# Optimization experiments

Hardware: AMD Instinct MI355X
Metric: run time of the kernel (lower is better)

## Reference

```python
import jax, jax.numpy as jnp
import numpy as np

N_NODES = 50000
NEG_SLOPE = 0.2


def _gat_conv(x, src, dst, W, a_src, a_dst, b, num_nodes):
    # x: [N, F_in]; src/dst: [E'] (self-loops already appended)
    H, C = a_src.shape
    h = (x @ W).reshape(num_nodes, H, C)            # [N, H, C]
    al_s = (h * a_src).sum(-1)                      # [N, H]
    al_d = (h * a_dst).sum(-1)                      # [N, H]
    e = jax.nn.leaky_relu(al_s[src] + al_d[dst], NEG_SLOPE)  # [E', H]
    # segment softmax over incoming edges of each destination node
    e_max = jax.ops.segment_max(e, dst, num_segments=num_nodes)
    e_max = jnp.where(jnp.isfinite(e_max), e_max, 0.0)
    ex = jnp.exp(e - e_max[dst])
    denom = jax.ops.segment_sum(ex, dst, num_segments=num_nodes)
    alpha = ex / (denom[dst] + 1e-16)               # [E', H]
    msg = h[src] * alpha[:, :, None]                # [E', H, C]
    out = jax.ops.segment_sum(msg, dst, num_segments=num_nodes)  # [N, H, C]
    return out.reshape(num_nodes, H * C) + b


def _glorot(key, shape):
    fan_in, fan_out = shape[0], shape[-1]
    std = np.sqrt(2.0 / (fan_in + fan_out)).astype(np.float32)
    return jax.random.normal(key, shape, dtype=jnp.float32) * std


def setup_inputs() -> dict:
    key = jax.random.key(0)
    ks = jax.random.split(key, 16)
    N, F_in, Hid, Cls, H = N_NODES, 128, 128, 40, 8
    C = Hid // H  # 16
    inp = {
        "x": jax.random.normal(ks[0], (N, F_in), dtype=jnp.float32),
        "edge_index": jax.random.randint(ks[1], (2, 800000), 0, N, dtype=jnp.int32),
        # layer 0: F_in -> H x C
        "W0": _glorot(ks[2], (F_in, H * C)),
        "as0": _glorot(ks[3], (H, C)),
        "ad0": _glorot(ks[4], (H, C)),
        "b0": jnp.zeros((H * C,), dtype=jnp.float32),
        # layer 1: Hid -> H x C
        "W1": _glorot(ks[5], (Hid, H * C)),
        "as1": _glorot(ks[6], (H, C)),
        "ad1": _glorot(ks[7], (H, C)),
        "b1": jnp.zeros((H * C,), dtype=jnp.float32),
        "W2": _glorot(ks[8], (Hid, Cls)),
        "as2": _glorot(ks[9], (1, Cls)),
        "ad2": _glorot(ks[10], (1, Cls)),
        "b2": jnp.zeros((Cls,), dtype=jnp.float32),
    }
    return inp


def reference(x, edge_index, W0, as0, ad0, b0, W1, as1, ad1, b1, W2, as2, ad2, b2):
    N = x.shape[0]
    loop = jnp.arange(N, dtype=edge_index.dtype)
    src = jnp.concatenate([edge_index[0], loop])  # add self-loops (PyG default)
    dst = jnp.concatenate([edge_index[1], loop])
    h = _gat_conv(x, src, dst, W0, as0, ad0, b0, N)
    h = jax.nn.relu(h)                      # dropout is identity in eval mode
    h = _gat_conv(h, src, dst, W1, as1, ad1, b1, N)
    h = jax.nn.relu(h)
    out = _gat_conv(h, src, dst, W2, as2, ad2, b2, N)  # [N, n_classes]
    return out
```

## Files before the change

kernel.cpp:

```cpp
#include <hip/hip_runtime.h>

#define NN    50000
#define ERAW  800000
#define ETOT  850000
#define NBUCK 782
#define EBR   1280
#define EPB_A 4096
#define NBLK_A ((ETOT + EPB_A - 1) / EPB_A)
#define NCNT  (NBUCK * 64)

typedef __attribute__((ext_vector_type(8))) short bf16x8;
typedef __attribute__((ext_vector_type(4))) float f32x4;

union U16x8 { uint4 u; bf16x8 s; };
__device__ __forceinline__ bf16x8 as_bf(uint4 v) { U16x8 t; t.u = v; return t.s; }

__device__ __forceinline__ void edge_sd(const int* __restrict__ ei, int e, int& s, int& d) {
    if (e < ERAW) { s = ei[e]; d = ei[ERAW + e]; }
    else { int n = e - ERAW; s = n; d = n; }
}

__device__ __forceinline__ unsigned pack_bf16x2(float a, float b) {
    unsigned ua = __float_as_uint(a), ub = __float_as_uint(b);
    ua += 0x7fffu + ((ua >> 16) & 1u);
    ub += 0x7fffu + ((ub >> 16) & 1u);
    return (ua >> 16) | (ub & 0xffff0000u);
}
__device__ __forceinline__ float2 unpack_bf16x2(unsigned v) {
    float2 r;
    r.x = __uint_as_float(v << 16);
    r.y = __uint_as_float(v & 0xffff0000u);
    return r;
}

__global__ void prep_misc(const float* __restrict__ W0, const float* __restrict__ W1,
                          const float* __restrict__ W2,
                          const float* __restrict__ as0, const float* __restrict__ ad0,
                          const float* __restrict__ as1, const float* __restrict__ ad1,
                          const float* __restrict__ as2, const float* __restrict__ ad2,
                          unsigned* __restrict__ Wbp0, unsigned* __restrict__ Wbp1,
                          unsigned* __restrict__ Wadp0, unsigned* __restrict__ Wadp1,
                          float* __restrict__ W2e, int* __restrict__ cursor) {
    int g = blockIdx.x * 256 + threadIdx.x;
    if (g < 4096) {
        int which = g >> 11;
        int r = g & 2047;
        int ct = r >> 8, kc = (r >> 6) & 3, l = r & 63;
        int lr = l & 15, lg = l >> 4;
        int col = ct * 16 + lr, k0 = kc * 32 + lg * 8;
        const float* W = which ? W1 : W0;
        unsigned* O = which ? Wbp1 : Wbp0;
        uint4 o;
        o.x = pack_bf16x2(W[(k0 + 0) * 128 + col], W[(k0 + 1) * 128 + col]);
        o.y = pack_bf16x2(W[(k0 + 2) * 128 + col], W[(k0 + 3) * 128 + col]);
        o.z = pack_bf16x2(W[(k0 + 4) * 128 + col], W[(k0 + 5) * 128 + col]);
        o.w = pack_bf16x2(W[(k0 + 6) * 128 + col], W[(k0 + 7) * 128 + col]);
        ((uint4*)O)[(ct * 4 + kc) * 64 + l] = o;
    } else if (g < 4608) {
        int gg = g - 4096;
        int which = gg >> 8;
        int r = gg & 255;
        int kc = r >> 6, l = r & 63;
        int lr = l & 15, lg = l >> 4;
        const float* W = which ? W1 : W0;
        const float* av = (lr < 8) ? (which ? as1 : as0) : (which ? ad1 : ad0);
        unsigned* O = which ? Wadp1 : Wadp0;
        int h = lr & 7;
        int k0 = kc * 32 + lg * 8;
        float v[8];
        #pragma unroll
        for (int j = 0; j < 8; ++j) {
            float s = 0.f;
            #pragma unroll
            for (int c = 0; c < 16; ++c) s += W[(k0 + j) * 128 + h * 16 + c] * av[h * 16 + c];
            v[j] = s;
        }
        uint4 o;
        o.x = pack_bf16x2(v[0], v[1]);
        o.y = pack_bf16x2(v[2], v[3]);
        o.z = pack_bf16x2(v[4], v[5]);
        o.w = pack_bf16x2(v[6], v[7]);
        ((uint4*)O)[kc * 64 + l] = o;
    } else if (g < 4608 + 6144) {
        int gg = g - 4608;
        int k = gg / 48, j = gg - k * 48;
        float v = 0.f;
        if (j < 40) v = W2[k * 40 + j];
        else if (j == 40) { for (int c = 0; c < 40; ++c) v += W2[k * 40 + c] * as2[c]; }
        else if (j == 41) { for (int c = 0; c < 40; ++c) v += W2[k * 40 + c] * ad2[c]; }
        W2e[k * 48 + j] = v;
    } else if (g < 4608 + 6144 + NBUCK) {
        int b = g - 10752;
        cursor[b] = b * EBR;
    }
}

__global__ void conv_x(const float* __restrict__ x, unsigned* __restrict__ xb) {
    int g = blockIdx.x * 256 + threadIdx.x;
    if (g >= NN * 32) return;
    float4 v = ((const float4*)x)[g];
    uint2 o;
    o.x = pack_bf16x2(v.x, v.y);
    o.y = pack_bf16x2(v.z, v.w);
    ((uint2*)xb)[g] = o;
}

__global__ __launch_bounds__(256) void kA3(const int* __restrict__ ei, int* __restrict__ cursor,
                                           unsigned* __restrict__ ebkt) {
    __shared__ int lb[NBUCK];
    int t = threadIdx.x;
    for (int i = t; i < NBUCK; i += 256) lb[i] = 0;
    __syncthreads();
    int base = blockIdx.x * EPB_A;
    #pragma unroll 4
    for (int k = 0; k < EPB_A / 256; ++k) {
        int e = base + k * 256 + t;
        if (e < ETOT) {
            int s, d; edge_sd(ei, e, s, d); (void)s;
            atomicAdd(&lb[d >> 6], 1);
        }
    }
    __syncthreads();
    for (int i = t; i < NBUCK; i += 256) {
        int c = lb[i];
        lb[i] = c ? atomicAdd(&cursor[i], c) : 0;
    }
    __syncthreads();
    #pragma unroll 4
    for (int k = 0; k < EPB_A / 256; ++k) {
        int e = base + k * 256 + t;
        if (e < ETOT) {
            int s, d; edge_sd(ei, e, s, d);
            int b = d >> 6;
            int pos = atomicAdd(&lb[b], 1);
            if (pos < (b + 1) * EBR)
                ebkt[pos] = ((unsigned)d << 16) | (unsigned)s;
        }
    }
}

__global__ __launch_bounds__(256) void kB(const int* __restrict__ cursor,
                                          const unsigned* __restrict__ ebkt,
                                          int* __restrict__ row_start, int* __restrict__ row_end,
                                          unsigned short* __restrict__ src_u16) {
    __shared__ int lc[64];
    int b = blockIdx.x, t = threadIdx.x;
    if (t < 64) lc[t] = 0;
    __syncthreads();
    int s0 = b * EBR;
    int s1 = cursor[b]; if (s1 > s0 + EBR) s1 = s0 + EBR;
    for (int i = s0 + t; i < s1; i += 256) atomicAdd(&lc[(ebkt[i] >> 16) & 63], 1);
    __syncthreads();
    if (t < 64) {
        int v = lc[t];
        int inc = v;
        #pragma unroll
        for (int off = 1; off < 64; off <<= 1) {
            int u = __shfl_up(inc, off);
            if (t >= off) inc += u;
        }
        int st = s0 + inc - v;
        row_start[b * 64 + t] = st;
        row_end[b * 64 + t] = st + v;
        lc[t] = st;
    }
    __syncthreads();
    for (int i = s0 + t; i < s1; i += 256) {
        unsigned k = ebkt[i];
        int pos = atomicAdd(&lc[(k >> 16) & 63], 1);
        src_u16[pos] = (unsigned short)(k & 0xffffu);
    }
}

__global__ __launch_bounds__(256) void gemm_mfma128(
    const uint4* __restrict__ xb, const uint4* __restrict__ Wbp,
    const uint4* __restrict__ Wadp, unsigned* __restrict__ hb,
    float* __restrict__ als, float* __restrict__ ald)
{
    int t = threadIdx.x;
    int wv = t >> 6, l = t & 63;
    int lr = l & 15, lg = l >> 4;
    int n0 = blockIdx.x * 64 + wv * 16;
    int nodeA = n0 + lr; if (nodeA >= NN) nodeA = NN - 1;
    const uint4* xr = xb + (size_t)nodeA * 16;
    uint4 a0 = xr[0 * 4 + lg];
    uint4 a1 = xr[1 * 4 + lg];
    uint4 a2 = xr[2 * 4 + lg];
    uint4 a3 = xr[3 * 4 + lg];
    #pragma unroll
    for (int ct = 0; ct < 8; ++ct) {
        const uint4* bp = Wbp + (size_t)(ct * 4) * 64;
        uint4 b0 = bp[0 * 64 + l];
        uint4 b1 = bp[1 * 64 + l];
        uint4 b2 = bp[2 * 64 + l];
        uint4 b3 = bp[3 * 64 + l];
        f32x4 acc = {0.f, 0.f, 0.f, 0.f};
        acc = __builtin_amdgcn_mfma_f32_16x16x32_bf16(as_bf(a0), as_bf(b0), acc, 0, 0, 0);
        acc = __builtin_amdgcn_mfma_f32_16x16x32_bf16(as_bf(a1), as_bf(b1), acc, 0, 0, 0);
        acc = __builtin_amdgcn_mfma_f32_16x16x32_bf16(as_bf(a2), as_bf(b2), acc, 0, 0, 0);
        acc = __builtin_amdgcn_mfma_f32_16x16x32_bf16(as_bf(a3), as_bf(b3), acc, 0, 0, 0);
        #pragma unroll
        for (int j = 0; j < 4; ++j) {
            float hv = acc[j];
            float nbv = __shfl_xor(hv, 1);
            int node = n0 + lg * 4 + j;
            if ((lr & 1) == 0 && node < NN)
                hb[(size_t)node * 64 + ct * 8 + (lr >> 1)] = pack_bf16x2(hv, nbv);
        }
    }
    {
        uint4 b0 = Wadp[0 * 64 + l];
        uint4 b1 = Wadp[1 * 64 + l];
        uint4 b2 = Wadp[2 * 64 + l];
        uint4 b3 = Wadp[3 * 64 + l];
        f32x4 acc = {0.f, 0.f, 0.f, 0.f};
        acc = __builtin_amdgcn_mfma_f32_16x16x32_bf16(as_bf(a0), as_bf(b0), acc, 0, 0, 0);
        acc = __builtin_amdgcn_mfma_f32_16x16x32_bf16(as_bf(a1), as_bf(b1), acc, 0, 0, 0);
        acc = __builtin_amdgcn_mfma_f32_16x16x32_bf16(as_bf(a2), as_bf(b2), acc, 0, 0, 0);
        acc = __builtin_amdgcn_mfma_f32_16x16x32_bf16(as_bf(a3), as_bf(b3), acc, 0, 0, 0);
        #pragma unroll
        for (int j = 0; j < 4; ++j) {
            int node = n0 + lg * 4 + j;
            if (node < NN) {
                if (lr < 8) als[node * 8 + lr] = acc[j];
                else        ald[node * 8 + (lr - 8)] = acc[j];
            }
        }
    }
}

__global__ __launch_bounds__(256) void gemm_att40(
    const unsigned* __restrict__ fb, const float* __restrict__ W2e,
    unsigned* __restrict__ hb40, float* __restrict__ als, float* __restrict__ ald)
{
    __shared__ float ws[128 * 48];
    __shared__ unsigned xs[16 * 64];
    int t = threadIdx.x;
    int n0 = blockIdx.x * 16;
    #pragma unroll
    for (int i = 0; i < 6; ++i) ((float4*)ws)[i * 256 + t] = ((const float4*)W2e)[i * 256 + t];
    ((uint4*)xs)[t] = ((const uint4*)fb)[(size_t)n0 * 16 + t];
    __syncthreads();
    int w = t >> 6, c = t & 63;
    int cc = c < 42 ? c : 41;
    float acc[4] = {0.f, 0.f, 0.f, 0.f};
    #pragma unroll 4
    for (int kc = 0; kc < 32; ++kc) {
        float w0 = ws[(kc * 4 + 0) * 48 + cc];
        float w1 = ws[(kc * 4 + 1) * 48 + cc];
        float w2 = ws[(kc * 4 + 2) * 48 + cc];
        float w3 = ws[(kc * 4 + 3) * 48 + cc];
        #pragma unroll
        for (int i = 0; i < 4; ++i) {
            float2 f0 = unpack_bf16x2(xs[(4 * w + i) * 64 + kc * 2]);
            float2 f1 = unpack_bf16x2(xs[(4 * w + i) * 64 + kc * 2 + 1]);
            acc[i] = fmaf(f0.x, w0, acc[i]);
            acc[i] = fmaf(f0.y, w1, acc[i]);
            acc[i] = fmaf(f1.x, w2, acc[i]);
            acc[i] = fmaf(f1.y, w3, acc[i]);
        }
    }
    #pragma unroll
    for (int i = 0; i < 4; ++i) {
        int n = n0 + 4 * w + i;
        float nb = __shfl_xor(acc[i], 1);
        if ((c & 1) == 0 && c < 40) hb40[(size_t)n * 32 + (c >> 1)] = pack_bf16x2(acc[i], nb);
        if (c == 40) als[n] = acc[i];
        if (c == 41) ald[n] = acc[i];
    }
}

template<bool RELU>
__global__ void dst_agg128(const int* __restrict__ row_start, const int* __restrict__ row_end,
                           const unsigned short* __restrict__ src_u16,
                           const float* __restrict__ als, const float* __restrict__ ald,
                           const unsigned* __restrict__ hb, const float* __restrict__ bias,
                           unsigned* __restrict__ outb)
{
    int wp = (blockIdx.x * blockDim.x + threadIdx.x) >> 6;
    if (wp >= NN / 4) return;
    int lane = threadIdx.x & 63;
    int q = lane >> 4, l = lane & 15;
    int node = 4 * wp + q;
    int myh = l >> 1;
    float aldv = ald[node * 8 + myh];
    int i = row_start[node], end = row_end[node];
    float4 accA = make_float4(0.f, 0.f, 0.f, 0.f);
    float4 accB = make_float4(0.f, 0.f, 0.f, 0.f);
    float den = 0.f;
    while (__any(i + 4 <= end)) {
        if (i + 4 <= end) {
            int s0 = src_u16[i], s1 = src_u16[i + 1], s2 = src_u16[i + 2], s3 = src_u16[i + 3];
            float e0 = als[s0 * 8 + myh] + aldv;
            float e1 = als[s1 * 8 + myh] + aldv;
            float e2 = als[s2 * 8 + myh] + aldv;
            float e3 = als[s3 * 8 + myh] + aldv;
            uint4 p0 = ((const uint4*)(hb + (size_t)s0 * 64))[l];
            uint4 p1 = ((const uint4*)(hb + (size_t)s1 * 64))[l];
            uint4 p2 = ((const uint4*)(hb + (size_t)s2 * 64))[l];
            uint4 p3 = ((const uint4*)(hb + (size_t)s3 * 64))[l];
            e0 = e0 > 0.f ? e0 : 0.2f * e0;
            e1 = e1 > 0.f ? e1 : 0.2f * e1;
            e2 = e2 > 0.f ? e2 : 0.2f * e2;
            e3 = e3 > 0.f ? e3 : 0.2f * e3;
            float a0 = __expf(e0), a1 = __expf(e1), a2 = __expf(e2), a3 = __expf(e3);
            den += (a0 + a1) + (a2 + a3);
            float2 t0, t1;
            t0 = unpack_bf16x2(p0.x); t1 = unpack_bf16x2(p0.y);
            accA.x = fmaf(t0.x, a0, accA.x); accA.y = fmaf(t0.y, a0, accA.y);
            accA.z = fmaf(t1.x, a0, accA.z); accA.w = fmaf(t1.y, a0, accA.w);
            t0 = unpack_bf16x2(p0.z); t1 = unpack_bf16x2(p0.w);
            accB.x = fmaf(t0.x, a0, accB.x); accB.y = fmaf(t0.y, a0, accB.y);
            accB.z = fmaf(t1.x, a0, accB.z); accB.w = fmaf(t1.y, a0, accB.w);
            t0 = unpack_bf16x2(p1.x); t1 = unpack_bf16x2(p1.y);
            accA.x = fmaf(t0.x, a1, accA.x); accA.y = fmaf(t0.y, a1, accA.y);
            accA.z = fmaf(t1.x, a1, accA.z); accA.w = fmaf(t1.y, a1, accA.w);
            t0 = unpack_bf16x2(p1.z); t1 = unpack_bf16x2(p1.w);
            accB.x = fmaf(t0.x, a1, accB.x); accB.y = fmaf(t0.y, a1, accB.y);
            accB.z = fmaf(t1.x, a1, accB.z); accB.w = fmaf(t1.y, a1, accB.w);
            t0 = unpack_bf16x2(p2.x); t1 = unpack_bf16x2(p2.y);
            accA.x = fmaf(t0.x, a2, accA.x); accA.y = fmaf(t0.y, a2, accA.y);
            accA.z = fmaf(t1.x, a2, accA.z); accA.w = fmaf(t1.y, a2, accA.w);
            t0 = unpack_bf16x2(p2.z); t1 = unpack_bf16x2(p2.w);
            accB.x = fmaf(t0.x, a2, accB.x); accB.y = fmaf(t0.y, a2, accB.y);
            accB.z = fmaf(t1.x, a2, accB.z); accB.w = fmaf(t1.y, a2, accB.w);
            t0 = unpack_bf16x2(p3.x); t1 = unpack_bf16x2(p3.y);
            accA.x = fmaf(t0.x, a3, accA.x); accA.y = fmaf(t0.y, a3, accA.y);
            accA.z = fmaf(t1.x, a3, accA.z); accA.w = fmaf(t1.y, a3, accA.w);
            t0 = unpack_bf16x2(p3.z); t1 = unpack_bf16x2(p3.w);
            accB.x = fmaf(t0.x, a3, accB.x); accB.y = fmaf(t0.y, a3, accB.y);
            accB.z = fmaf(t1.x, a3, accB.z); accB.w = fmaf(t1.y, a3, accB.w);
            i += 4;
        }
    }
    while (__any(i < end)) {
        if (i < end) {
            int s0 = src_u16[i];
            float e0 = als[s0 * 8 + myh] + aldv;
            e0 = e0 > 0.f ? e0 : 0.2f * e0;
            float a0 = __expf(e0);
            den += a0;
            uint4 p0 = ((const uint4*)(hb + (size_t)s0 * 64))[l];
            float2 t0 = unpack_bf16x2(p0.x), t1 = unpack_bf16x2(p0.y);
            accA.x = fmaf(t0.x, a0, accA.x); accA.y = fmaf(t0.y, a0, accA.y);
            accA.z = fmaf(t1.x, a0, accA.z); accA.w = fmaf(t1.y, a0, accA.w);
            t0 = unpack_bf16x2(p0.z); t1 = unpack_bf16x2(p0.w);
            accB.x = fmaf(t0.x, a0, accB.x); accB.y = fmaf(t0.y, a0, accB.y);
            accB.z = fmaf(t1.x, a0, accB.z); accB.w = fmaf(t1.y, a0, accB.w);
            ++i;
        }
    }
    float inv = 1.f / (den + 1e-16f);
    float4 bvA = ((const float4*)bias)[2 * l];
    float4 bvB = ((const float4*)bias)[2 * l + 1];
    float4 oA, oB;
    oA.x = accA.x * inv + bvA.x; oA.y = accA.y * inv + bvA.y;
    oA.z = accA.z * inv + bvA.z; oA.w = accA.w * inv + bvA.w;
    oB.x = accB.x * inv + bvB.x; oB.y = accB.y * inv + bvB.y;
    oB.z = accB.z * inv + bvB.z; oB.w = accB.w * inv + bvB.w;
    if (RELU) {
        oA.x = fmaxf(oA.x, 0.f); oA.y = fmaxf(oA.y, 0.f);
        oA.z = fmaxf(oA.z, 0.f); oA.w = fmaxf(oA.w, 0.f);
        oB.x = fmaxf(oB.x, 0.f); oB.y = fmaxf(oB.y, 0.f);
        oB.z = fmaxf(oB.z, 0.f); oB.w = fmaxf(oB.w, 0.f);
    }
    uint4 ob;
    ob.x = pack_bf16x2(oA.x, oA.y);
    ob.y = pack_bf16x2(oA.z, oA.w);
    ob.z = pack_bf16x2(oB.x, oB.y);
    ob.w = pack_bf16x2(oB.z, oB.w);
    ((uint4*)(outb + (size_t)node * 64))[l] = ob;
}

__global__ void dst_agg40(const int* __restrict__ row_start, const int* __restrict__ row_end,
                          const unsigned short* __restrict__ src_u16,
                          const float* __restrict__ als, const float* __restrict__ ald,
                          const unsigned* __restrict__ hb40, const float* __restrict__ bias,
                          float* __restrict__ out)
{
    int wp = (blockIdx.x * blockDim.x + threadIdx.x) >> 6;
    if (wp >= NN / 4) return;
    int lane = threadIdx.x & 63;
    int q = lane >> 4, l = lane & 15;
    int node = 4 * wp + q;
    float aldv = ald[node];
    int i = row_start[node], end = row_end[node];
    float4 acc = make_float4(0.f, 0.f, 0.f, 0.f);
    float den = 0.f;
    while (__any(i + 4 <= end)) {
        if (i + 4 <= end) {
            int s0 = src_u16[i], s1 = src_u16[i + 1], s2 = src_u16[i + 2], s3 = src_u16[i + 3];
            float e0 = als[s0] + aldv;
            float e1 = als[s1] + aldv;
            float e2 = als[s2] + aldv;
            float e3 = als[s3] + aldv;
            uint2 p0 = ((const uint2*)(hb40 + (size_t)s0 * 32))[l];
            uint2 p1 = ((const uint2*)(hb40 + (size_t)s1 * 32))[l];
            uint2 p2 = ((const uint2*)(hb40 + (size_t)s2 * 32))[l];
            uint2 p3 = ((const uint2*)(hb40 + (size_t)s3 * 32))[l];
            e0 = e0 > 0.f ? e0 : 0.2f * e0;
            e1 = e1 > 0.f ? e1 : 0.2f * e1;
            e2 = e2 > 0.f ? e2 : 0.2f * e2;
            e3 = e3 > 0.f ? e3 : 0.2f * e3;
            float b0 = __expf(e0), b1 = __expf(e1), b2 = __expf(e2), b3 = __expf(e3);
            den += (b0 + b1) + (b2 + b3);
            float2 u0 = unpack_bf16x2(p0.x), v0 = unpack_bf16x2(p0.y);
            float2 u1 = unpack_bf16x2(p1.x), v1 = unpack_bf16x2(p1.y);
            float2 u2 = unpack_bf16x2(p2.x), v2 = unpack_bf16x2(p2.y);
            float2 u3 = unpack_bf16x2(p3.x), v3 = unpack_bf16x2(p3.y);
            acc.x = fmaf(u0.x, b0, acc.x); acc.y = fmaf(u0.y, b0, acc.y);
            acc.z = fmaf(v0.x, b0, acc.z); acc.w = fmaf(v0.y, b0, acc.w);
            acc.x = fmaf(u1.x, b1, acc.x); acc.y = fmaf(u1.y, b1, acc.y);
            acc.z = fmaf(v1.x, b1, acc.z); acc.w = fmaf(v1.y, b1, acc.w);
            acc.x = fmaf(u2.x, b2, acc.x); acc.y = fmaf(u2.y, b2, acc.y);
            acc.z = fmaf(v2.x, b2, acc.z); acc.w = fmaf(v2.y, b2, acc.w);
            acc.x = fmaf(u3.x, b3, acc.x); acc.y = fmaf(u3.y, b3, acc.y);
            acc.z = fmaf(v3.x, b3, acc.z); acc.w = fmaf(v3.y, b3, acc.w);
            i += 4;
        }
    }
    while (__any(i < end)) {
        if (i < end) {
            int s0 = src_u16[i];
            float e0 = als[s0] + aldv;
            e0 = e0 > 0.f ? e0 : 0.2f * e0;
            float b0 = __expf(e0);
            den += b0;
            uint2 p0 = ((const uint2*)(hb40 + (size_t)s0 * 32))[l];
            float2 u0 = unpack_bf16x2(p0.x), v0 = unpack_bf16x2(p0.y);
            acc.x = fmaf(u0.x, b0, acc.x); acc.y = fmaf(u0.y, b0, acc.y);
            acc.z = fmaf(v0.x, b0, acc.z); acc.w = fmaf(v0.y, b0, acc.w);
            ++i;
        }
    }
    if (l < 10) {
        float inv = 1.f / (den + 1e-16f);
        float4 bv = ((const float4*)bias)[l];
        float4 o;
        o.x = acc.x * inv + bv.x;
        o.y = acc.y * inv + bv.y;
        o.z = acc.z * inv + bv.z;
        o.w = acc.w * inv + bv.w;
        ((float4*)(out + (size_t)node * 40))[l] = o;
    }
}

extern "C" void kernel_launch(void* const* d_in, const int* in_sizes, int n_in,
                              void* d_out, int out_size, void* d_ws, size_t ws_size,
                              hipStream_t stream) {
    const float* x   = (const float*)d_in[0];
    const int*   ei  = (const int*)d_in[1];
    const float* W0  = (const float*)d_in[2];
    const float* as0 = (const float*)d_in[3];
    const float* ad0 = (const float*)d_in[4];
    const float* b0  = (const float*)d_in[5];
    const float* W1  = (const float*)d_in[6];
    const float* as1 = (const float*)d_in[7];
    const float* ad1 = (const float*)d_in[8];
    const float* b1  = (const float*)d_in[9];
    const float* W2  = (const float*)d_in[10];
    const float* as2 = (const float*)d_in[11];
    const float* ad2 = (const float*)d_in[12];
    const float* b2  = (const float*)d_in[13];
    float* out = (float*)d_out;

    float* ws = (float*)d_ws;
    size_t off = 0;
    unsigned* hb   = (unsigned*)(ws + off); off += (size_t)NN * 64;
    unsigned* xb   = (unsigned*)(ws + off); off += (size_t)NN * 64;
    unsigned* fAb  = (unsigned*)(ws + off); off += (size_t)NN * 64;
    unsigned* fBb  = (unsigned*)(ws + off); off += (size_t)NN * 64;
    unsigned* hb40 = (unsigned*)(ws + off); off += (size_t)NN * 32;
    float* als     = ws + off; off += (size_t)NN * 8;
    float* ald     = ws + off; off += (size_t)NN * 8;
    unsigned* Wbp0 = (unsigned*)(ws + off); off += 8192;
    unsigned* Wbp1 = (unsigned*)(ws + off); off += 8192;
    unsigned* Wadp0 = (unsigned*)(ws + off); off += 1024;
    unsigned* Wadp1 = (unsigned*)(ws + off); off += 1024;
    float* W2e     = ws + off; off += 128 * 48;
    int* ibase      = (int*)(ws + off);
    int* cursor     = ibase; ibase += NBUCK;
    int* row_start  = ibase; ibase += NCNT;
    int* row_end    = ibase; ibase += NCNT;
    unsigned* ebkt  = (unsigned*)ibase; ibase += NBUCK * EBR;
    unsigned short* src_u16 = (unsigned short*)ibase;

    const int TB = 256;

    prep_misc<<<46, 256, 0, stream>>>(W0, W1, W2, as0, ad0, as1, ad1, as2, ad2,
                                      Wbp0, Wbp1, Wadp0, Wadp1, W2e, cursor);
    kA3<<<NBLK_A, 256, 0, stream>>>(ei, cursor, ebkt);
    kB<<<NBUCK, 256, 0, stream>>>(cursor, ebkt, row_start, row_end, src_u16);
    conv_x<<<(NN * 32 + TB - 1) / TB, TB, 0, stream>>>(x, xb);

    const int GGM   = (NN + 63) / 64;
    const int GG40  = NN / 16;
    const int GAGG4 = ((NN / 4) * 64 + TB - 1) / TB;

    gemm_mfma128<<<GGM, 256, 0, stream>>>((const uint4*)xb, (const uint4*)Wbp0,
                                          (const uint4*)Wadp0, hb, als, ald);
    dst_agg128<true><<<GAGG4, TB, 0, stream>>>(row_start, row_end, src_u16, als, ald, hb, b0, fAb);

    gemm_mfma128<<<GGM, 256, 0, stream>>>((const uint4*)fAb, (const uint4*)Wbp1,
                                          (const uint4*)Wadp1, hb, als, ald);
    dst_agg128<true><<<GAGG4, TB, 0, stream>>>(row_start, row_end, src_u16, als, ald, hb, b1, fBb);

    gemm_att40<<<GG40, 256, 0, stream>>>(fBb, W2e, hb40, als, ald);
    dst_agg40<<<GAGG4, TB, 0, stream>>>(row_start, row_end, src_u16, als, ald, hb40, b2, out);
}
```

Measured before the change: 189.6 us.

## Split edges across half-waves in aggregation, fold log2e into attention weights, merge conv_x

```diff
diff --git a/kernel.cpp b/kernel.cpp
--- a/kernel.cpp
+++ b/kernel.cpp
@@ -8,6 +8,7 @@
 #define EPB_A 4096
 #define NBLK_A ((ETOT + EPB_A - 1) / EPB_A)
 #define NCNT  (NBUCK * 64)
+#define INV_LN2 1.4426950408889634f
 
 typedef __attribute__((ext_vector_type(8))) short bf16x8;
 typedef __attribute__((ext_vector_type(4))) float f32x4;
@@ -33,14 +34,26 @@
     return r;
 }
 
-__global__ void prep_misc(const float* __restrict__ W0, const float* __restrict__ W1,
+__global__ void prep_conv(const float* __restrict__ x,
+                          const float* __restrict__ W0, const float* __restrict__ W1,
                           const float* __restrict__ W2,
                           const float* __restrict__ as0, const float* __restrict__ ad0,
                           const float* __restrict__ as1, const float* __restrict__ ad1,
                           const float* __restrict__ as2, const float* __restrict__ ad2,
                           unsigned* __restrict__ Wbp0, unsigned* __restrict__ Wbp1,
                           unsigned* __restrict__ Wadp0, unsigned* __restrict__ Wadp1,
-                          float* __restrict__ W2e, int* __restrict__ cursor) {
+                          float* __restrict__ W2e, int* __restrict__ cursor,
+                          unsigned* __restrict__ xb) {
+    if (blockIdx.x >= 46) {
+        int g = (blockIdx.x - 46) * 256 + threadIdx.x;
+        if (g >= NN * 32) return;
+        float4 v = ((const float4*)x)[g];
+        uint2 o;
+        o.x = pack_bf16x2(v.x, v.y);
+        o.y = pack_bf16x2(v.z, v.w);
+        ((uint2*)xb)[g] = o;
+        return;
+    }
     int g = blockIdx.x * 256 + threadIdx.x;
     if (g < 4096) {
         int which = g >> 11;
@@ -73,7 +86,7 @@
             float s = 0.f;
             #pragma unroll
             for (int c = 0; c < 16; ++c) s += W[(k0 + j) * 128 + h * 16 + c] * av[h * 16 + c];
-            v[j] = s;
+            v[j] = s * INV_LN2;
         }
         uint4 o;
         o.x = pack_bf16x2(v[0], v[1]);
@@ -86,23 +99,13 @@
         int k = gg / 48, j = gg - k * 48;
         float v = 0.f;
         if (j < 40) v = W2[k * 40 + j];
-        else if (j == 40) { for (int c = 0; c < 40; ++c) v += W2[k * 40 + c] * as2[c]; }
-        else if (j == 41) { for (int c = 0; c < 40; ++c) v += W2[k * 40 + c] * ad2[c]; }
+        else if (j == 40) { for (int c = 0; c < 40; ++c) v += W2[k * 40 + c] * as2[c]; v *= INV_LN2; }
+        else if (j == 41) { for (int c = 0; c < 40; ++c) v += W2[k * 40 + c] * ad2[c]; v *= INV_LN2; }
         W2e[k * 48 + j] = v;
     } else if (g < 4608 + 6144 + NBUCK) {
         int b = g - 10752;
         cursor[b] = b * EBR;
     }
-}
-
-__global__ void conv_x(const float* __restrict__ x, unsigned* __restrict__ xb) {
-    int g = blockIdx.x * 256 + threadIdx.x;
-    if (g >= NN * 32) return;
-    float4 v = ((const float4*)x)[g];
-    uint2 o;
-    o.x = pack_bf16x2(v.x, v.y);
-    o.y = pack_bf16x2(v.z, v.w);
-    ((uint2*)xb)[g] = o;
 }
 
 __global__ __launch_bounds__(256) void kA3(const int* __restrict__ ei, int* __restrict__ cursor,
@@ -270,178 +273,143 @@
     }
 }
 
+#define AGG128_BODY(IDX) { \
+    int idx = (IDX); \
+    bool v = idx < end; \
+    int s = v ? (int)src_u16[idx] : 0; \
+    float e = als[s * 8 + m] + aldv; \
+    e = e > 0.f ? e : 0.2f * e; \
+    float a = v ? exp2f(e) : 0.f; \
+    den += a; \
+    const uint4* hr = (const uint4*)(hb + (size_t)s * 64) + 2 * m; \
+    uint4 p0 = hr[0], p1 = hr[1]; \
+    float2 t_; \
+    t_ = unpack_bf16x2(p0.x); acc[0] = fmaf(t_.x, a, acc[0]); acc[1] = fmaf(t_.y, a, acc[1]); \
+    t_ = unpack_bf16x2(p0.y); acc[2] = fmaf(t_.x, a, acc[2]); acc[3] = fmaf(t_.y, a, acc[3]); \
+    t_ = unpack_bf16x2(p0.z); acc[4] = fmaf(t_.x, a, acc[4]); acc[5] = fmaf(t_.y, a, acc[5]); \
+    t_ = unpack_bf16x2(p0.w); acc[6] = fmaf(t_.x, a, acc[6]); acc[7] = fmaf(t_.y, a, acc[7]); \
+    t_ = unpack_bf16x2(p1.x); acc[8] = fmaf(t_.x, a, acc[8]); acc[9] = fmaf(t_.y, a, acc[9]); \
+    t_ = unpack_bf16x2(p1.y); acc[10] = fmaf(t_.x, a, acc[10]); acc[11] = fmaf(t_.y, a, acc[11]); \
+    t_ = unpack_bf16x2(p1.z); acc[12] = fmaf(t_.x, a, acc[12]); acc[13] = fmaf(t_.y, a, acc[13]); \
+    t_ = unpack_bf16x2(p1.w); acc[14] = fmaf(t_.x, a, acc[14]); acc[15] = fmaf(t_.y, a, acc[15]); }
+
 template<bool RELU>
-__global__ void dst_agg128(const int* __restrict__ row_start, const int* __restrict__ row_end,
-                           const unsigned short* __restrict__ src_u16,
-                           const float* __restrict__ als, const float* __restrict__ ald,
-                           const unsigned* __restrict__ hb, const float* __restrict__ bias,
-                           unsigned* __restrict__ outb)
+__global__ __launch_bounds__(256) void dst_agg128(
+    const int* __restrict__ row_start, const int* __restrict__ row_end,
+    const unsigned short* __restrict__ src_u16,
+    const float* __restrict__ als, const float* __restrict__ ald,
+    const unsigned* __restrict__ hb, const float* __restrict__ bias,
+    unsigned* __restrict__ outb)
 {
     int wp = (blockIdx.x * blockDim.x + threadIdx.x) >> 6;
     if (wp >= NN / 4) return;
     int lane = threadIdx.x & 63;
     int q = lane >> 4, l = lane & 15;
+    int sub = l >> 3, m = l & 7;
     int node = 4 * wp + q;
-    int myh = l >> 1;
-    float aldv = ald[node * 8 + myh];
+    float aldv = ald[node * 8 + m];
     int i = row_start[node], end = row_end[node];
-    float4 accA = make_float4(0.f, 0.f, 0.f, 0.f);
-    float4 accB = make_float4(0.f, 0.f, 0.f, 0.f);
+    float acc[16];
+    #pragma unroll
+    for (int k = 0; k < 16; ++k) acc[k] = 0.f;
     float den = 0.f;
-    while (__any(i + 4 <= end)) {
-        if (i + 4 <= end) {
-            int s0 = src_u16[i], s1 = src_u16[i + 1], s2 = src_u16[i + 2], s3 = src_u16[i + 3];
-            float e0 = als[s0 * 8 + myh] + aldv;
-            float e1 = als[s1 * 8 + myh] + aldv;
-            float e2 = als[s2 * 8 + myh] + aldv;
-            float e3 = als[s3 * 8 + myh] + aldv;
-            uint4 p0 = ((const uint4*)(hb + (size_t)s0 * 64))[l];
-            uint4 p1 = ((const uint4*)(hb + (size_t)s1 * 64))[l];
-            uint4 p2 = ((const uint4*)(hb + (size_t)s2 * 64))[l];
-            uint4 p3 = ((const uint4*)(hb + (size_t)s3 * 64))[l];
-            e0 = e0 > 0.f ? e0 : 0.2f * e0;
-            e1 = e1 > 0.f ? e1 : 0.2f * e1;
-            e2 = e2 > 0.f ? e2 : 0.2f * e2;
-            e3 = e3 > 0.f ? e3 : 0.2f * e3;
-            float a0 = __expf(e0), a1 = __expf(e1), a2 = __expf(e2), a3 = __expf(e3);
-            den += (a0 + a1) + (a2 + a3);
-            float2 t0, t1;
-            t0 = unpack_bf16x2(p0.x); t1 = unpack_bf16x2(p0.y);
-            accA.x = fmaf(t0.x, a0, accA.x); accA.y = fmaf(t0.y, a0, accA.y);
-            accA.z = fmaf(t1.x, a0, accA.z); accA.w = fmaf(t1.y, a0, accA.w);
-            t0 = unpack_bf16x2(p0.z); t1 = unpack_bf16x2(p0.w);
-            accB.x = fmaf(t0.x, a0, accB.x); accB.y = fmaf(t0.y, a0, accB.y);
-            accB.z = fmaf(t1.x, a0, accB.z); accB.w = fmaf(t1.y, a0, accB.w);
-            t0 = unpack_bf16x2(p1.x); t1 = unpack_bf16x2(p1.y);
-            accA.x = fmaf(t0.x, a1, accA.x); accA.y = fmaf(t0.y, a1, accA.y);
-            accA.z = fmaf(t1.x, a1, accA.z); accA.w = fmaf(t1.y, a1, accA.w);
-            t0 = unpack_bf16x2(p1.z); t1 = unpack_bf16x2(p1.w);
-            accB.x = fmaf(t0.x, a1, accB.x); accB.y = fmaf(t0.y, a1, accB.y);
-            accB.z = fmaf(t1.x, a1, accB.z); accB.w = fmaf(t1.y, a1, accB.w);
-            t0 = unpack_bf16x2(p2.x); t1 = unpack_bf16x2(p2.y);
-            accA.x = fmaf(t0.x, a2, accA.x); accA.y = fmaf(t0.y, a2, accA.y);
-            accA.z = fmaf(t1.x, a2, accA.z); accA.w = fmaf(t1.y, a2, accA.w);
-            t0 = unpack_bf16x2(p2.z); t1 = unpack_bf16x2(p2.w);
-            accB.x = fmaf(t0.x, a2, accB.x); accB.y = fmaf(t0.y, a2, accB.y);
-            accB.z = fmaf(t1.x, a2, accB.z); accB.w = fmaf(t1.y, a2, accB.w);
-            t0 = unpack_bf16x2(p3.x); t1 = unpack_bf16x2(p3.y);
-            accA.x = fmaf(t0.x, a3, accA.x); accA.y = fmaf(t0.y, a3, accA.y);
-            accA.z = fmaf(t1.x, a3, accA.z); accA.w = fmaf(t1.y, a3, accA.w);
-            t0 = unpack_bf16x2(p3.z); t1 = unpack_bf16x2(p3.w);
-            accB.x = fmaf(t0.x, a3, accB.x); accB.y = fmaf(t0.y, a3, accB.y);
-            accB.z = fmaf(t1.x, a3, accB.z); accB.w = fmaf(t1.y, a3, accB.w);
-            i += 4;
-        }
+    while (__any(i + 2 < end)) {
+        AGG128_BODY(i + sub)
+        AGG128_BODY(i + 2 + sub)
+        i += 4;
     }
     while (__any(i < end)) {
-        if (i < end) {
-            int s0 = src_u16[i];
-            float e0 = als[s0 * 8 + myh] + aldv;
-            e0 = e0 > 0.f ? e0 : 0.2f * e0;
-            float a0 = __expf(e0);
-            den += a0;
-            uint4 p0 = ((const uint4*)(hb + (size_t)s0 * 64))[l];
-            float2 t0 = unpack_bf16x2(p0.x), t1 = unpack_bf16x2(p0.y);
-            accA.x = fmaf(t0.x, a0, accA.x); accA.y = fmaf(t0.y, a0, accA.y);
-            accA.z = fmaf(t1.x, a0, accA.z); accA.w = fmaf(t1.y, a0, accA.w);
-            t0 = unpack_bf16x2(p0.z); t1 = unpack_bf16x2(p0.w);
-            accB.x = fmaf(t0.x, a0, accB.x); accB.y = fmaf(t0.y, a0, accB.y);
-            accB.z = fmaf(t1.x, a0, accB.z); accB.w = fmaf(t1.y, a0, accB.w);
-            ++i;
-        }
-    }
-    float inv = 1.f / (den + 1e-16f);
-    float4 bvA = ((const float4*)bias)[2 * l];
-    float4 bvB = ((const float4*)bias)[2 * l + 1];
-    float4 oA, oB;
-    oA.x = accA.x * inv + bvA.x; oA.y = accA.y * inv + bvA.y;
-    oA.z = accA.z * inv + bvA.z; oA.w = accA.w * inv + bvA.w;
-    oB.x = accB.x * inv + bvB.x; oB.y = accB.y * inv + bvB.y;
-    oB.z = accB.z * inv + bvB.z; oB.w = accB.w * inv + bvB.w;
-    if (RELU) {
-        oA.x = fmaxf(oA.x, 0.f); oA.y = fmaxf(oA.y, 0.f);
-        oA.z = fmaxf(oA.z, 0.f); oA.w = fmaxf(oA.w, 0.f);
-        oB.x = fmaxf(oB.x, 0.f); oB.y = fmaxf(oB.y, 0.f);
-        oB.z = fmaxf(oB.z, 0.f); oB.w = fmaxf(oB.w, 0.f);
-    }
-    uint4 ob;
-    ob.x = pack_bf16x2(oA.x, oA.y);
-    ob.y = pack_bf16x2(oA.z, oA.w);
-    ob.z = pack_bf16x2(oB.x, oB.y);
-    ob.w = pack_bf16x2(oB.z, oB.w);
-    ((uint4*)(outb + (size_t)node * 64))[l] = ob;
-}
-
-__global__ void dst_agg40(const int* __restrict__ row_start, const int* __restrict__ row_end,
-                          const unsigned short* __restrict__ src_u16,
-                          const float* __restrict__ als, const float* __restrict__ ald,
-                          const unsigned* __restrict__ hb40, const float* __restrict__ bias,
-                          float* __restrict__ out)
+        AGG128_BODY(i + sub)
+        i += 2;
+    }
+    den += __shfl_xor(den, 8);
+    #pragma unroll
+    for (int k = 0; k < 16; ++k) acc[k] += __shfl_xor(acc[k], 8);
+    if (sub == 0) {
+        float inv = 1.f / (den + 1e-16f);
+        const float4* b4 = (const float4*)bias;
+        float o[16];
+        #pragma unroll
+        for (int k = 0; k < 4; ++k) {
+            float4 bv = b4[4 * m + k];
+            o[4 * k + 0] = acc[4 * k + 0] * inv + bv.x;
+            o[4 * k + 1] = acc[4 * k + 1] * inv + bv.y;
+            o[4 * k + 2] = acc[4 * k + 2] * inv + bv.z;
+            o[4 * k + 3] = acc[4 * k + 3] * inv + bv.w;
+        }
+        if (RELU) {
+            #pragma unroll
+            for (int k = 0; k < 16; ++k) o[k] = fmaxf(o[k], 0.f);
+        }
+        uint4 ob0, ob1;
+        ob0.x = pack_bf16x2(o[0], o[1]);  ob0.y = pack_bf16x2(o[2], o[3]);
+        ob0.z = pack_bf16x2(o[4], o[5]);  ob0.w = pack_bf16x2(o[6], o[7]);
+        ob1.x = pack_bf16x2(o[8], o[9]);  ob1.y = pack_bf16x2(o[10], o[11]);
+        ob1.z = pack_bf16x2(o[12], o[13]); ob1.w = pack_bf16x2(o[14], o[15]);
+        uint4* orow = (uint4*)(outb + (size_t)node * 64);
+        orow[2 * m] = ob0;
+        orow[2 * m + 1] = ob1;
+    }
+}
+
+#define AGG40_BODY(IDX) { \
+    int idx = (IDX); \
+    bool v = idx < end; \
+    int s = v ? (int)src_u16[idx] : 0; \
+    float e = als[s] + aldv; \
+    e = e > 0.f ? e : 0.2f * e; \
+    float a = v ? exp2f(e) : 0.f; \
+    den += a; \
+    uint4 p = ((const uint4*)(hb40 + (size_t)s * 32))[m]; \
+    float2 t_; \
+    t_ = unpack_bf16x2(p.x); acc[0] = fmaf(t_.x, a, acc[0]); acc[1] = fmaf(t_.y, a, acc[1]); \
+    t_ = unpack_bf16x2(p.y); acc[2] = fmaf(t_.x, a, acc[2]); acc[3] = fmaf(t_.y, a, acc[3]); \
+    t_ = unpack_bf16x2(p.z); acc[4] = fmaf(t_.x, a, acc[4]); acc[5] = fmaf(t_.y, a, acc[5]); \
+    t_ = unpack_bf16x2(p.w); acc[6] = fmaf(t_.x, a, acc[6]); acc[7] = fmaf(t_.y, a, acc[7]); }
+
+__global__ __launch_bounds__(256) void dst_agg40(
+    const int* __restrict__ row_start, const int* __restrict__ row_end,
+    const unsigned short* __restrict__ src_u16,
+    const float* __restrict__ als, const float* __restrict__ ald,
+    const unsigned* __restrict__ hb40, const float* __restrict__ bias,
+    float* __restrict__ out)
 {
     int wp = (blockIdx.x * blockDim.x + threadIdx.x) >> 6;
     if (wp >= NN / 4) return;
     int lane = threadIdx.x & 63;
     int q = lane >> 4, l = lane & 15;
+    int sub = l >> 3, m = l & 7;
     int node = 4 * wp + q;
     float aldv = ald[node];
     int i = row_start[node], end = row_end[node];
-    float4 acc = make_float4(0.f, 0.f, 0.f, 0.f);
+    float acc[8];
+    #pragma unroll
+    for (int k = 0; k < 8; ++k) acc[k] = 0.f;
     float den = 0.f;
-    while (__any(i + 4 <= end)) {
-        if (i + 4 <= end) {
-            int s0 = src_u16[i], s1 = src_u16[i + 1], s2 = src_u16[i + 2], s3 = src_u16[i + 3];
-            float e0 = als[s0] + aldv;
-            float e1 = als[s1] + aldv;
-            float e2 = als[s2] + aldv;
-            float e3 = als[s3] + aldv;
-            uint2 p0 = ((const uint2*)(hb40 + (size_t)s0 * 32))[l];
-            uint2 p1 = ((const uint2*)(hb40 + (size_t)s1 * 32))[l];
-            uint2 p2 = ((const uint2*)(hb40 + (size_t)s2 * 32))[l];
-            uint2 p3 = ((const uint2*)(hb40 + (size_t)s3 * 32))[l];
-            e0 = e0 > 0.f ? e0 : 0.2f * e0;
-            e1 = e1 > 0.f ? e1 : 0.2f * e1;
-            e2 = e2 > 0.f ? e2 : 0.2f * e2;
-            e3 = e3 > 0.f ? e3 : 0.2f * e3;
-            float b0 = __expf(e0), b1 = __expf(e1), b2 = __expf(e2), b3 = __expf(e3);
-            den += (b0 + b1) + (b2 + b3);
-            float2 u0 = unpack_bf16x2(p0.x), v0 = unpack_bf16x2(p0.y);
-            float2 u1 = unpack_bf16x2(p1.x), v1 = unpack_bf16x2(p1.y);
-            float2 u2 = unpack_bf16x2(p2.x), v2 = unpack_bf16x2(p2.y);
-            float2 u3 = unpack_bf16x2(p3.x), v3 = unpack_bf16x2(p3.y);
-            acc.x = fmaf(u0.x, b0, acc.x); acc.y = fmaf(u0.y, b0, acc.y);
-            acc.z = fmaf(v0.x, b0, acc.z); acc.w = fmaf(v0.y, b0, acc.w);
-            acc.x = fmaf(u1.x, b1, acc.x); acc.y = fmaf(u1.y, b1, acc.y);
-            acc.z = fmaf(v1.x, b1, acc.z); acc.w = fmaf(v1.y, b1, acc.w);
-            acc.x = fmaf(u2.x, b2, acc.x); acc.y = fmaf(u2.y, b2, acc.y);
-            acc.z = fmaf(v2.x, b2, acc.z); acc.w = fmaf(v2.y, b2, acc.w);
-            acc.x = fmaf(u3.x, b3, acc.x); acc.y = fmaf(u3.y, b3, acc.y);
-            acc.z = fmaf(v3.x, b3, acc.z); acc.w = fmaf(v3.y, b3, acc.w);
-            i += 4;
-        }
+    while (__any(i + 2 < end)) {
+        AGG40_BODY(i + sub)
+        AGG40_BODY(i + 2 + sub)
+        i += 4;
     }
     while (__any(i < end)) {
-        if (i < end) {
-            int s0 = src_u16[i];
-            float e0 = als[s0] + aldv;
-            e0 = e0 > 0.f ? e0 : 0.2f * e0;
-            float b0 = __expf(e0);
-            den += b0;
-            uint2 p0 = ((const uint2*)(hb40 + (size_t)s0 * 32))[l];
-            float2 u0 = unpack_bf16x2(p0.x), v0 = unpack_bf16x2(p0.y);
-            acc.x = fmaf(u0.x, b0, acc.x); acc.y = fmaf(u0.y, b0, acc.y);
-            acc.z = fmaf(v0.x, b0, acc.z); acc.w = fmaf(v0.y, b0, acc.w);
-            ++i;
-        }
-    }
-    if (l < 10) {
+        AGG40_BODY(i + sub)
+        i += 2;
+    }
+    den += __shfl_xor(den, 8);
+    #pragma unroll
+    for (int k = 0; k < 8; ++k) acc[k] += __shfl_xor(acc[k], 8);
+    if (sub == 0 && m < 5) {
         float inv = 1.f / (den + 1e-16f);
-        float4 bv = ((const float4*)bias)[l];
-        float4 o;
-        o.x = acc.x * inv + bv.x;
-        o.y = acc.y * inv + bv.y;
-        o.z = acc.z * inv + bv.z;
-        o.w = acc.w * inv + bv.w;
-        ((float4*)(out + (size_t)node * 40))[l] = o;
+        const float4* b4 = (const float4*)bias;
+        float4 bv0 = b4[2 * m], bv1 = b4[2 * m + 1];
+        float4 o0, o1;
+        o0.x = acc[0] * inv + bv0.x; o0.y = acc[1] * inv + bv0.y;
+        o0.z = acc[2] * inv + bv0.z; o0.w = acc[3] * inv + bv0.w;
+        o1.x = acc[4] * inv + bv1.x; o1.y = acc[5] * inv + bv1.y;
+        o1.z = acc[6] * inv + bv1.z; o1.w = acc[7] * inv + bv1.w;
+        float4* orow = (float4*)(out + (size_t)node * 40);
+        orow[2 * m] = o0;
+        orow[2 * m + 1] = o1;
     }
 }
 
@@ -487,11 +455,11 @@
 
     const int TB = 256;
 
-    prep_misc<<<46, 256, 0, stream>>>(W0, W1, W2, as0, ad0, as1, ad1, as2, ad2,
-                                      Wbp0, Wbp1, Wadp0, Wadp1, W2e, cursor);
+    prep_conv<<<46 + (NN * 32 + TB - 1) / TB, TB, 0, stream>>>(
+        x, W0, W1, W2, as0, ad0, as1, ad1, as2, ad2,
+        Wbp0, Wbp1, Wadp0, Wadp1, W2e, cursor, xb);
     kA3<<<NBLK_A, 256, 0, stream>>>(ei, cursor, ebkt);
     kB<<<NBUCK, 256, 0, stream>>>(cursor, ebkt, row_start, row_end, src_u16);
-    conv_x<<<(NN * 32 + TB - 1) / TB, TB, 0, stream>>>(x, xb);
 
     const int GGM   = (NN + 63) / 64;
     const int GG40  = NN / 16;
@@ -502,7 +470,7 @@
     dst_agg128<true><<<GAGG4, TB, 0, stream>>>(row_start, row_end, src_u16, als, ald, hb, b0, fAb);
 
     gemm_mfma128<<<GGM, 256, 0, stream>>>((const uint4*)fAb, (const uint4*)Wbp1,
-                                          (const uint4*)Wadp1, hb, als, ald);
+                                          (const uint4*)Wbp1 == 0 ? 0 : (const uint4*)Wadp1, hb, als, ald);
     dst_agg128<true><<<GAGG4, TB, 0, stream>>>(row_start, row_end, src_u16, als, ald, hb, b1, fBb);
 
     gemm_att40<<<GG40, 256, 0, stream>>>(fBb, W2e, hb40, als, ald);
```

New measurement: 195.6 us. 3.2% more time.

## Sort destination nodes by degree for balanced aggregation, use exp2 with prescaled logits

Applied to the files above, without the earlier changes.

```diff
diff --git a/kernel.cpp b/kernel.cpp
--- a/kernel.cpp
+++ b/kernel.cpp
@@ -8,6 +8,7 @@
 #define EPB_A 4096
 #define NBLK_A ((ETOT + EPB_A - 1) / EPB_A)
 #define NCNT  (NBUCK * 64)
+#define INV_LN2 1.4426950408889634f
 
 typedef __attribute__((ext_vector_type(8))) short bf16x8;
 typedef __attribute__((ext_vector_type(4))) float f32x4;
@@ -33,14 +34,26 @@
     return r;
 }
 
-__global__ void prep_misc(const float* __restrict__ W0, const float* __restrict__ W1,
+__global__ void prep_conv(const float* __restrict__ x,
+                          const float* __restrict__ W0, const float* __restrict__ W1,
                           const float* __restrict__ W2,
                           const float* __restrict__ as0, const float* __restrict__ ad0,
                           const float* __restrict__ as1, const float* __restrict__ ad1,
                           const float* __restrict__ as2, const float* __restrict__ ad2,
                           unsigned* __restrict__ Wbp0, unsigned* __restrict__ Wbp1,
                           unsigned* __restrict__ Wadp0, unsigned* __restrict__ Wadp1,
-                          float* __restrict__ W2e, int* __restrict__ cursor) {
+                          float* __restrict__ W2e, int* __restrict__ cursor,
+                          int* __restrict__ gbins, unsigned* __restrict__ xb) {
+    if (blockIdx.x >= 46) {
+        int g = (blockIdx.x - 46) * 256 + threadIdx.x;
+        if (g >= NN * 32) return;
+        float4 v = ((const float4*)x)[g];
+        uint2 o;
+        o.x = pack_bf16x2(v.x, v.y);
+        o.y = pack_bf16x2(v.z, v.w);
+        ((uint2*)xb)[g] = o;
+        return;
+    }
     int g = blockIdx.x * 256 + threadIdx.x;
     if (g < 4096) {
         int which = g >> 11;
@@ -73,7 +86,7 @@
             float s = 0.f;
             #pragma unroll
             for (int c = 0; c < 16; ++c) s += W[(k0 + j) * 128 + h * 16 + c] * av[h * 16 + c];
-            v[j] = s;
+            v[j] = s * INV_LN2;
         }
         uint4 o;
         o.x = pack_bf16x2(v[0], v[1]);
@@ -86,23 +99,15 @@
         int k = gg / 48, j = gg - k * 48;
         float v = 0.f;
         if (j < 40) v = W2[k * 40 + j];
-        else if (j == 40) { for (int c = 0; c < 40; ++c) v += W2[k * 40 + c] * as2[c]; }
-        else if (j == 41) { for (int c = 0; c < 40; ++c) v += W2[k * 40 + c] * ad2[c]; }
+        else if (j == 40) { for (int c = 0; c < 40; ++c) v += W2[k * 40 + c] * as2[c]; v *= INV_LN2; }
+        else if (j == 41) { for (int c = 0; c < 40; ++c) v += W2[k * 40 + c] * ad2[c]; v *= INV_LN2; }
         W2e[k * 48 + j] = v;
-    } else if (g < 4608 + 6144 + NBUCK) {
+    } else if (g < 10752 + NBUCK) {
         int b = g - 10752;
         cursor[b] = b * EBR;
-    }
-}
-
-__global__ void conv_x(const float* __restrict__ x, unsigned* __restrict__ xb) {
-    int g = blockIdx.x * 256 + threadIdx.x;
-    if (g >= NN * 32) return;
-    float4 v = ((const float4*)x)[g];
-    uint2 o;
-    o.x = pack_bf16x2(v.x, v.y);
-    o.y = pack_bf16x2(v.z, v.w);
-    ((uint2*)xb)[g] = o;
+    } else if (g < 10752 + NBUCK + 64) {
+        gbins[g - 10752 - NBUCK] = 0;
+    }
 }
 
 __global__ __launch_bounds__(256) void kA3(const int* __restrict__ ei, int* __restrict__ cursor,
@@ -142,6 +147,7 @@
 __global__ __launch_bounds__(256) void kB(const int* __restrict__ cursor,
                                           const unsigned* __restrict__ ebkt,
                                           int* __restrict__ row_start, int* __restrict__ row_end,
+                                          int* __restrict__ gbins,
                                           unsigned short* __restrict__ src_u16) {
     __shared__ int lc[64];
     int b = blockIdx.x, t = threadIdx.x;
@@ -163,6 +169,7 @@
         row_start[b * 64 + t] = st;
         row_end[b * 64 + t] = st + v;
         lc[t] = st;
+        if (b * 64 + t < NN) atomicAdd(&gbins[v < 63 ? v : 63], 1);
     }
     __syncthreads();
     for (int i = s0 + t; i < s1; i += 256) {
@@ -170,6 +177,28 @@
         int pos = atomicAdd(&lc[(k >> 16) & 63], 1);
         src_u16[pos] = (unsigned short)(k & 0xffffu);
     }
+}
+
+__global__ void k_degscan(const int* __restrict__ gbins, int* __restrict__ gcur) {
+    int t = threadIdx.x;
+    int v = gbins[t];
+    int inc = v;
+    #pragma unroll
+    for (int off = 1; off < 64; off <<= 1) {
+        int u = __shfl_up(inc, off);
+        if (t >= off) inc += u;
+    }
+    gcur[t] = inc - v;
+}
+
+__global__ void k_degscatter(const int* __restrict__ row_start, const int* __restrict__ row_end,
+                             int* __restrict__ gcur, int* __restrict__ perm) {
+    int n = blockIdx.x * 256 + threadIdx.x;
+    if (n >= NN) return;
+    int deg = row_end[n] - row_start[n];
+    if (deg > 63) deg = 63;
+    int pos = atomicAdd(&gcur[deg], 1);
+    perm[pos] = n;
 }
 
 __global__ __launch_bounds__(256) void gemm_mfma128(
@@ -271,7 +300,8 @@
 }
 
 template<bool RELU>
-__global__ void dst_agg128(const int* __restrict__ row_start, const int* __restrict__ row_end,
+__global__ void dst_agg128(const int* __restrict__ perm,
+                           const int* __restrict__ row_start, const int* __restrict__ row_end,
                            const unsigned short* __restrict__ src_u16,
                            const float* __restrict__ als, const float* __restrict__ ald,
                            const unsigned* __restrict__ hb, const float* __restrict__ bias,
@@ -281,7 +311,7 @@
     if (wp >= NN / 4) return;
     int lane = threadIdx.x & 63;
     int q = lane >> 4, l = lane & 15;
-    int node = 4 * wp + q;
+    int node = perm[4 * wp + q];
     int myh = l >> 1;
     float aldv = ald[node * 8 + myh];
     int i = row_start[node], end = row_end[node];
@@ -303,7 +333,7 @@
             e1 = e1 > 0.f ? e1 : 0.2f * e1;
             e2 = e2 > 0.f ? e2 : 0.2f * e2;
             e3 = e3 > 0.f ? e3 : 0.2f * e3;
-            float a0 = __expf(e0), a1 = __expf(e1), a2 = __expf(e2), a3 = __expf(e3);
+            float a0 = exp2f(e0), a1 = exp2f(e1), a2 = exp2f(e2), a3 = exp2f(e3);
             den += (a0 + a1) + (a2 + a3);
             float2 t0, t1;
             t0 = unpack_bf16x2(p0.x); t1 = unpack_bf16x2(p0.y);
@@ -338,7 +368,7 @@
             int s0 = src_u16[i];
             float e0 = als[s0 * 8 + myh] + aldv;
             e0 = e0 > 0.f ? e0 : 0.2f * e0;
-            float a0 = __expf(e0);
+            float a0 = exp2f(e0);
             den += a0;
             uint4 p0 = ((const uint4*)(hb + (size_t)s0 * 64))[l];
             float2 t0 = unpack_bf16x2(p0.x), t1 = unpack_bf16x2(p0.y);
@@ -372,7 +402,8 @@
     ((uint4*)(outb + (size_t)node * 64))[l] = ob;
 }
 
-__global__ void dst_agg40(const int* __restrict__ row_start, const int* __restrict__ row_end,
+__global__ void dst_agg40(const int* __restrict__ perm,
+                          const int* __restrict__ row_start, const int* __restrict__ row_end,
                           const unsigned short* __restrict__ src_u16,
                           const float* __restrict__ als, const float* __restrict__ ald,
                           const unsigned* __restrict__ hb40, const float* __restrict__ bias,
@@ -382,7 +413,7 @@
     if (wp >= NN / 4) return;
     int lane = threadIdx.x & 63;
     int q = lane >> 4, l = lane & 15;
-    int node = 4 * wp + q;
+    int node = perm[4 * wp + q];
     float aldv = ald[node];
     int i = row_start[node], end = row_end[node];
     float4 acc = make_float4(0.f, 0.f, 0.f, 0.f);
@@ -402,7 +433,7 @@
             e1 = e1 > 0.f ? e1 : 0.2f * e1;
             e2 = e2 > 0.f ? e2 : 0.2f * e2;
             e3 = e3 > 0.f ? e3 : 0.2f * e3;
-            float b0 = __expf(e0), b1 = __expf(e1), b2 = __expf(e2), b3 = __expf(e3);
+            float b0 = exp2f(e0), b1 = exp2f(e1), b2 = exp2f(e2), b3 = exp2f(e3);
             den += (b0 + b1) + (b2 + b3);
             float2 u0 = unpack_bf16x2(p0.x), v0 = unpack_bf16x2(p0.y);
             float2 u1 = unpack_bf16x2(p1.x), v1 = unpack_bf16x2(p1.y);
@@ -424,7 +455,7 @@
             int s0 = src_u16[i];
             float e0 = als[s0] + aldv;
             e0 = e0 > 0.f ? e0 : 0.2f * e0;
-            float b0 = __expf(e0);
+            float b0 = exp2f(e0);
             den += b0;
             uint2 p0 = ((const uint2*)(hb40 + (size_t)s0 * 32))[l];
             float2 u0 = unpack_bf16x2(p0.x), v0 = unpack_bf16x2(p0.y);
@@ -482,16 +513,21 @@
     int* cursor     = ibase; ibase += NBUCK;
     int* row_start  = ibase; ibase += NCNT;
     int* row_end    = ibase; ibase += NCNT;
+    int* gbins      = ibase; ibase += 64;
+    int* gcur       = ibase; ibase += 64;
+    int* perm       = ibase; ibase += NN;
     unsigned* ebkt  = (unsigned*)ibase; ibase += NBUCK * EBR;
     unsigned short* src_u16 = (unsigned short*)ibase;
 
     const int TB = 256;
 
-    prep_misc<<<46, 256, 0, stream>>>(W0, W1, W2, as0, ad0, as1, ad1, as2, ad2,
-                                      Wbp0, Wbp1, Wadp0, Wadp1, W2e, cursor);
+    prep_conv<<<46 + (NN * 32 + TB - 1) / TB, TB, 0, stream>>>(
+        x, W0, W1, W2, as0, ad0, as1, ad1, as2, ad2,
+        Wbp0, Wbp1, Wadp0, Wadp1, W2e, cursor, gbins, xb);
     kA3<<<NBLK_A, 256, 0, stream>>>(ei, cursor, ebkt);
-    kB<<<NBUCK, 256, 0, stream>>>(cursor, ebkt, row_start, row_end, src_u16);
-    conv_x<<<(NN * 32 + TB - 1) / TB, TB, 0, stream>>>(x, xb);
+    kB<<<NBUCK, 256, 0, stream>>>(cursor, ebkt, row_start, row_end, gbins, src_u16);
+    k_degscan<<<1, 64, 0, stream>>>(gbins, gcur);
+    k_degscatter<<<(NN + TB - 1) / TB, TB, 0, stream>>>(row_start, row_end, gcur, perm);
 
     const int GGM   = (NN + 63) / 64;
     const int GG40  = NN / 16;
@@ -499,12 +535,12 @@
 
     gemm_mfma128<<<GGM, 256, 0, stream>>>((const uint4*)xb, (const uint4*)Wbp0,
                                           (const uint4*)Wadp0, hb, als, ald);
-    dst_agg128<true><<<GAGG4, TB, 0, stream>>>(row_start, row_end, src_u16, als, ald, hb, b0, fAb);
+    dst_agg128<true><<<GAGG4, TB, 0, stream>>>(perm, row_start, row_end, src_u16, als, ald, hb, b0, fAb);
 
     gemm_mfma128<<<GGM, 256, 0, stream>>>((const uint4*)fAb, (const uint4*)Wbp1,
                                           (const uint4*)Wadp1, hb, als, ald);
-    dst_agg128<true><<<GAGG4, TB, 0, stream>>>(row_start, row_end, src_u16, als, ald, hb, b1, fBb);
+    dst_agg128<true><<<GAGG4, TB, 0, stream>>>(perm, row_start, row_end, src_u16, als, ald, hb, b1, fBb);
 
     gemm_att40<<<GG40, 256, 0, stream>>>(fBb, W2e, hb40, als, ald);
-    dst_agg40<<<GAGG4, TB, 0, stream>>>(row_start, row_end, src_u16, als, ald, hb40, b2, out);
-}
+    dst_agg40<<<GAGG4, TB, 0, stream>>>(perm, row_start, row_end, src_u16, als, ald, hb40, b2, out);
+}
```

After: 426.9 us. 125% more time.
